# Performance work log

Measured on AMD Instinct MI355X. Metric: run time of the kernel, lower is better.

## Reference

```python
import jax, jax.numpy as jnp
import numpy as np

S, B, D_IN = 2048, 32, 512
H, PROJ, L = 1024, 512, 2
LN_EPS = 1e-5


def setup_inputs() -> dict:
    key = jax.random.key(0)
    ks = jax.random.split(key, 4)
    X = jax.random.normal(ks[0], (S, B, D_IN), dtype=jnp.float32)
    W = jax.random.normal(ks[1], (L, 3 * H, D_IN), dtype=jnp.float32) * (1.0 / np.sqrt(D_IN))
    b = jax.random.normal(ks[2], (L, 3 * H), dtype=jnp.float32) * 0.01
    P = jax.random.normal(ks[3], (L, PROJ, H), dtype=jnp.float32) * (1.0 / np.sqrt(H))
    gamma = jnp.ones((L, PROJ), dtype=jnp.float32)
    beta = jnp.zeros((L, PROJ), dtype=jnp.float32)
    return {"X": X, "W": W, "b": b, "P": P, "gamma": gamma, "beta": beta}


def _forget_mult(F, Z):
    # h_t = f_t * z_t + (1 - f_t) * h_{t-1}, h_0 = 0  (ForgetMult, hidden=None)
    def step(c, fz):
        f, z = fz
        c = f * z + (1.0 - f) * c
        return c, c
    c0 = jnp.zeros_like(Z[0])
    _, C = jax.lax.scan(step, c0, (F, Z))
    return C  # (S, B, H)


def _layer_norm(x, g, be):
    mu = jnp.mean(x, axis=-1, keepdims=True)
    var = jnp.mean(jnp.square(x - mu), axis=-1, keepdims=True)
    return (x - mu) * jax.lax.rsqrt(var + LN_EPS) * g + be


def reference(X, W, b, P, gamma, beta):
    inp = X
    last_states = []
    for i in range(L):
        # linear: (S,B,in) @ (in,3H) + b  -> gates
        Y = jnp.einsum('sbd,gd->sbg', inp, W[i]) + b[i]
        Z, F, O = jnp.split(Y, 3, axis=-1)
        Z = jnp.tanh(Z)
        F = jax.nn.sigmoid(F)
        C = _forget_mult(F, Z)                      # (S,B,H)
        Hout = jax.nn.sigmoid(O) * C                # output gate (QRNN-fo)
        inp = jnp.einsum('sbh,ph->sbp', Hout, P[i])  # projection, no bias
        inp = _layer_norm(inp, gamma[i], beta[i])
        last_states.append(C[-1])                   # (B,H)
    next_hidden = jnp.stack(last_states, axis=0)     # (L,B,H)
    return inp, next_hidden
```

## Files before the change

kernel.cpp:

```cpp
#include <hip/hip_runtime.h>
#include <hip/hip_bf16.h>

typedef _Float16 f16x8 __attribute__((ext_vector_type(8)));
typedef _Float16 f16x4 __attribute__((ext_vector_type(4)));
typedef float f32x4 __attribute__((ext_vector_type(4)));

#define SEQ 2048
#define BATCH 32
#define DIN 512
#define HID 1024
#define PROJ 512
#define ROWS (SEQ*BATCH)
#define G3H (3*HID)
#define NSEG 16
#define NCHAIN (BATCH*HID)

#define AS1(p) ((const __attribute__((address_space(1))) void*)(p))
#define AS3(p) ((__attribute__((address_space(3))) void*)(p))

__global__ __launch_bounds__(256)
void cvt_f32_f16(const float* __restrict__ in, _Float16* __restrict__ out, int n4)
{
    int i = blockIdx.x * 256 + threadIdx.x;
    if (i >= n4) return;
    float4 v = ((const float4*)in)[i];
    f16x4 o;
    o[0] = (_Float16)v.x; o[1] = (_Float16)v.y;
    o[2] = (_Float16)v.z; o[3] = (_Float16)v.w;
    ((f16x4*)out)[i] = o;
}

template<int MODE>
__global__ __launch_bounds__(256)
void gemm_lds(const _Float16* __restrict__ A, const _Float16* __restrict__ Bm,
              const float* __restrict__ bias, _Float16* __restrict__ C,
              int N, int K, int HH)
{
    __shared__ __align__(16) _Float16 sA[2][128][32];
    __shared__ __align__(16) _Float16 sB[2][128][32];

    const int tid  = threadIdx.x;
    const int lane = tid & 63;
    const int wave = tid >> 6;
    const int wm = wave >> 1;
    const int wn = wave & 1;
    const size_t row0 = (size_t)blockIdx.y * 128;
    const size_t col0 = (size_t)blockIdx.x * 128;

    const int crow = lane >> 2;
    const int ccol = (lane & 3) * 8;

    f32x4 acc[4][4] = {};

    const int rl = lane & 15;
    const int kb = (lane >> 4) * 8;
    const int nk = K / 32;

    const int c0 = wave * 2, c1 = wave * 2 + 1;
    const _Float16* gA0 = A  + (row0 + c0 * 16 + crow) * (size_t)K + ccol;
    const _Float16* gA1 = A  + (row0 + c1 * 16 + crow) * (size_t)K + ccol;
    const _Float16* gB0 = Bm + (col0 + c0 * 16 + crow) * (size_t)K + ccol;
    const _Float16* gB1 = Bm + (col0 + c1 * 16 + crow) * (size_t)K + ccol;

#define STAGE(buf, kt)                                                          \
    do {                                                                        \
        __builtin_amdgcn_global_load_lds(AS1(gA0 + (size_t)(kt) * 32),          \
                                         AS3(&sA[buf][c0 * 16][0]), 16, 0, 0);  \
        __builtin_amdgcn_global_load_lds(AS1(gB0 + (size_t)(kt) * 32),          \
                                         AS3(&sB[buf][c0 * 16][0]), 16, 0, 0);  \
        __builtin_amdgcn_global_load_lds(AS1(gA1 + (size_t)(kt) * 32),          \
                                         AS3(&sA[buf][c1 * 16][0]), 16, 0, 0);  \
        __builtin_amdgcn_global_load_lds(AS1(gB1 + (size_t)(kt) * 32),          \
                                         AS3(&sB[buf][c1 * 16][0]), 16, 0, 0);  \
    } while (0)

    int cur = 0;
    STAGE(0, 0);
    __syncthreads();

    for (int kt = 0; kt < nk; ++kt) {
        if (kt + 1 < nk) STAGE(cur ^ 1, kt + 1);
        f16x8 af[4], bf[4];
#pragma unroll
        for (int m = 0; m < 4; ++m)
            af[m] = *(const f16x8*)&sA[cur][wm * 64 + m * 16 + rl][kb];
#pragma unroll
        for (int n = 0; n < 4; ++n)
            bf[n] = *(const f16x8*)&sB[cur][wn * 64 + n * 16 + rl][kb];
#pragma unroll
        for (int m = 0; m < 4; ++m)
#pragma unroll
            for (int n = 0; n < 4; ++n)
                acc[m][n] = __builtin_amdgcn_mfma_f32_16x16x32_f16(af[m], bf[n], acc[m][n], 0, 0, 0);
        __syncthreads();
        cur ^= 1;
    }
#undef STAGE

#pragma unroll
    for (int m = 0; m < 4; ++m) {
#pragma unroll
        for (int n = 0; n < 4; ++n) {
            const size_t col = col0 + wn * 64 + n * 16 + rl;
            const size_t row = row0 + wm * 64 + m * 16 + (lane >> 4) * 4;
            float bv = (MODE == 0) ? bias[col] : 0.f;
#pragma unroll
            for (int j = 0; j < 4; ++j) {
                float v = acc[m][n][j];
                if (MODE == 0) {
                    v += bv;
                    if ((int)col < HH) {
                        float vc = fminf(fmaxf(v, -15.f), 15.f);
                        float e = __expf(2.f * vc);
                        v = __fdividef(e - 1.f, e + 1.f);
                    } else {
                        v = __fdividef(1.f, 1.f + __expf(-v));
                    }
                }
                C[(row + j) * (size_t)N + col] = (_Float16)v;
            }
        }
    }
}


__global__ __launch_bounds__(256)
void scan_p1(const _Float16* __restrict__ Y, float* __restrict__ Aseg,
             float* __restrict__ Bseg, int SL)
{
    const int t = blockIdx.x * 256 + threadIdx.x;
    const int g = blockIdx.y;
    const int h = t & (HID - 1);
    const int b = t >> 10;
    const _Float16* pz = Y + ((size_t)(g * SL) * BATCH + b) * G3H + h;
    const size_t strideY = (size_t)BATCH * G3H;
    float A = 1.f, Bv = 0.f;
#pragma unroll 4
    for (int k = 0; k < SL; ++k) {
        float z = (float)pz[0];
        float f = (float)pz[HID];
        Bv = f * z + (1.f - f) * Bv;
        A *= (1.f - f);
        pz += strideY;
    }
    Aseg[(size_t)g * NCHAIN + t] = A;
    Bseg[(size_t)g * NCHAIN + t] = Bv;
}

__global__ __launch_bounds__(256)
void scan_mid(const float* __restrict__ Aseg, const float* __restrict__ Bseg,
              float* __restrict__ cst, float* __restrict__ carry,
              float* __restrict__ hid, int first)
{
    const int t = blockIdx.x * 256 + threadIdx.x;
    float c = first ? 0.f : carry[t];
#pragma unroll
    for (int g = 0; g < NSEG; ++g) {
        cst[(size_t)g * NCHAIN + t] = c;
        c = Bseg[(size_t)g * NCHAIN + t] + Aseg[(size_t)g * NCHAIN + t] * c;
    }
    carry[t] = c;
    if (hid) hid[t] = c;
}

__global__ __launch_bounds__(256)
void scan_p2(const _Float16* __restrict__ Y, const float* __restrict__ cst,
             _Float16* __restrict__ Ho, int SL)
{
    const int t = blockIdx.x * 256 + threadIdx.x;
    const int g = blockIdx.y;
    const int h = t & (HID - 1);
    const int b = t >> 10;
    const _Float16* pz = Y + ((size_t)(g * SL) * BATCH + b) * G3H + h;
    _Float16* po = Ho + ((size_t)(g * SL) * BATCH + b) * HID + h;
    const size_t strideY = (size_t)BATCH * G3H;
    const size_t strideH = (size_t)BATCH * HID;
    float c = cst[(size_t)g * NCHAIN + t];
#pragma unroll 4
    for (int k = 0; k < SL; ++k) {
        float z = (float)pz[0];
        float f = (float)pz[HID];
        float o = (float)pz[2 * HID];
        c = f * z + (1.f - f) * c;
        *po = (_Float16)(o * c);
        pz += strideY;
        po += strideH;
    }
}

template<int OUT32>
__global__ __launch_bounds__(256)
void ln_kernel(const _Float16* __restrict__ Xin, const float* __restrict__ g,
               const float* __restrict__ be, _Float16* __restrict__ o16,
               float* __restrict__ o32)
{
    const int row  = blockIdx.x * 4 + (threadIdx.x >> 6);
    const int lane = threadIdx.x & 63;
    const _Float16* p = Xin + (size_t)row * PROJ + lane * 8;
    f16x8 v = *(const f16x8*)p;
    float x[8];
    float s = 0.f;
#pragma unroll
    for (int j = 0; j < 8; ++j) { x[j] = (float)v[j]; s += x[j]; }
#pragma unroll
    for (int d = 1; d < 64; d <<= 1) s += __shfl_xor(s, d);
    const float mu = s * (1.f / PROJ);
    float s2 = 0.f;
#pragma unroll
    for (int j = 0; j < 8; ++j) { float dd = x[j] - mu; s2 += dd * dd; }
#pragma unroll
    for (int d = 1; d < 64; d <<= 1) s2 += __shfl_xor(s2, d);
    const float rstd = rsqrtf(s2 * (1.f / PROJ) + 1e-5f);

    float y[8];
#pragma unroll
    for (int j = 0; j < 8; ++j)
        y[j] = (x[j] - mu) * rstd * g[lane * 8 + j] + be[lane * 8 + j];

    if (OUT32) {
        float* q = o32 + (size_t)row * PROJ + lane * 8;
        ((float4*)q)[0] = make_float4(y[0], y[1], y[2], y[3]);
        ((float4*)q)[1] = make_float4(y[4], y[5], y[6], y[7]);
    } else {
        f16x8 o;
#pragma unroll
        for (int j = 0; j < 8; ++j) o[j] = (_Float16)y[j];
        *(f16x8*)(o16 + (size_t)row * PROJ + lane * 8) = o;
    }
}

extern "C" void kernel_launch(void* const* d_in, const int* in_sizes, int n_in,
                              void* d_out, int out_size, void* d_ws, size_t ws_size,
                              hipStream_t stream)
{
    const float* X     = (const float*)d_in[0];
    const float* W     = (const float*)d_in[1];
    const float* b     = (const float*)d_in[2];
    const float* P     = (const float*)d_in[3];
    const float* gamma = (const float*)d_in[4];
    const float* beta  = (const float*)d_in[5];
    float* out = (float*)d_out;

    char* w = (char*)d_ws;
    _Float16* Xh = (_Float16*)w; w += (size_t)ROWS * DIN * 2;
    _Float16* Wh = (_Float16*)w; w += (size_t)2 * G3H * DIN * 2;
    _Float16* Ph = (_Float16*)w; w += (size_t)2 * PROJ * HID * 2;
    float* carry = (float*)w;    w += (size_t)NCHAIN * 4;
    float* Aseg  = (float*)w;    w += (size_t)NSEG * NCHAIN * 4;
    float* Bseg  = (float*)w;    w += (size_t)NSEG * NCHAIN * 4;
    float* cst   = (float*)w;    w += (size_t)NSEG * NCHAIN * 4;
    const size_t fixed = (size_t)(w - (char*)d_ws);

    const int cands[7] = {2048, 1024, 512, 256, 128, 64, 32};
    int CS = 32;
    for (int i = 0; i < 7; ++i) {
        size_t need = fixed + (size_t)cands[i] * 32 * (G3H + HID + PROJ) * 2;
        if (need <= ws_size) { CS = cands[i]; break; }
    }
    _Float16* Yg = (_Float16*)w; w += (size_t)CS * 32 * G3H * 2;
    _Float16* Ho = (_Float16*)w; w += (size_t)CS * 32 * HID * 2;
    _Float16* G2 = (_Float16*)w;

    cvt_f32_f16<<<(ROWS * DIN / 4 + 255) / 256, 256, 0, stream>>>(X, Xh, ROWS * DIN / 4);
    cvt_f32_f16<<<(2 * G3H * DIN / 4 + 255) / 256, 256, 0, stream>>>(W, Wh, 2 * G3H * DIN / 4);
    cvt_f32_f16<<<(2 * PROJ * HID / 4 + 255) / 256, 256, 0, stream>>>(P, Ph, 2 * PROJ * HID / 4);

    float* hid = out + (size_t)ROWS * PROJ;
    const int nch = SEQ / CS;
    const int rows = CS * BATCH;
    const int SL = CS / NSEG;

    for (int i = 0; i < 2; ++i) {
        for (int ch = 0; ch < nch; ++ch) {
            const size_t r0 = (size_t)ch * rows;
            gemm_lds<0><<<dim3(G3H / 128, rows / 128), 256, 0, stream>>>(
                Xh + r0 * DIN, Wh + (size_t)i * G3H * DIN, b + i * G3H, Yg, G3H, DIN, HID);
            scan_p1<<<dim3(NCHAIN / 256, NSEG), 256, 0, stream>>>(Yg, Aseg, Bseg, SL);
            scan_mid<<<NCHAIN / 256, 256, 0, stream>>>(
                Aseg, Bseg, cst, carry,
                (ch == nch - 1) ? hid + (size_t)i * NCHAIN : nullptr, ch == 0);
            scan_p2<<<dim3(NCHAIN / 256, NSEG), 256, 0, stream>>>(Yg, cst, Ho, SL);
            gemm_lds<1><<<dim3(PROJ / 128, rows / 128), 256, 0, stream>>>(
                Ho, Ph + (size_t)i * PROJ * HID, nullptr, G2, PROJ, HID, 0);
            if (i == 0)
                ln_kernel<0><<<rows / 4, 256, 0, stream>>>(G2, gamma, beta, Xh + r0 * PROJ, nullptr);
            else
                ln_kernel<1><<<rows / 4, 256, 0, stream>>>(G2, gamma + PROJ, beta + PROJ, nullptr, out + r0 * PROJ);
        }
    }
}
```

Baseline: 1.590 ms.

## Rework GEMM into 256x128 tiles with triple-buffered swizzled LDS pipeline

```diff
diff --git a/kernel.cpp b/kernel.cpp
--- a/kernel.cpp
+++ b/kernel.cpp
@@ -31,78 +31,117 @@
 }
 
 template<int MODE>
-__global__ __launch_bounds__(256)
+__global__ __launch_bounds__(512)
 void gemm_lds(const _Float16* __restrict__ A, const _Float16* __restrict__ Bm,
               const float* __restrict__ bias, _Float16* __restrict__ C,
               int N, int K, int HH)
 {
-    __shared__ __align__(16) _Float16 sA[2][128][32];
-    __shared__ __align__(16) _Float16 sB[2][128][32];
+    extern __shared__ __align__(16) char smem[];
+    char* sA = smem;
+    char* sB = smem + 98304;
 
     const int tid  = threadIdx.x;
     const int lane = tid & 63;
     const int wave = tid >> 6;
-    const int wm = wave >> 1;
-    const int wn = wave & 1;
-    const size_t row0 = (size_t)blockIdx.y * 128;
+    const int wm = wave & 3;
+    const int wn = wave >> 2;
+    const size_t row0 = (size_t)blockIdx.y * 256;
     const size_t col0 = (size_t)blockIdx.x * 128;
-
-    const int crow = lane >> 2;
-    const int ccol = (lane & 3) * 8;
+    const size_t Kb = (size_t)K * 2;
+
+    const char* Ab = (const char*)A;
+    const char* Bb = (const char*)Bm;
+
+    const int rl = lane & 15;
+    const int g  = lane >> 4;
+    const int swz = (rl & 7) << 4;
+    const int c0 = (g * 16) ^ swz;
+    const int c1 = (64 + g * 16) ^ swz;
+    const int aBase = (wm * 64 + rl) * 128;
+    const int bBase = (wn * 64 + rl) * 128;
+
+    const int srow = tid >> 3;
+    const int scb  = ((tid & 7) * 16) ^ ((srow & 7) << 4);
 
     f32x4 acc[4][4] = {};
-
-    const int rl = lane & 15;
-    const int kb = (lane >> 4) * 8;
-    const int nk = K / 32;
-
-    const int c0 = wave * 2, c1 = wave * 2 + 1;
-    const _Float16* gA0 = A  + (row0 + c0 * 16 + crow) * (size_t)K + ccol;
-    const _Float16* gA1 = A  + (row0 + c1 * 16 + crow) * (size_t)K + ccol;
-    const _Float16* gB0 = Bm + (col0 + c0 * 16 + crow) * (size_t)K + ccol;
-    const _Float16* gB1 = Bm + (col0 + c1 * 16 + crow) * (size_t)K + ccol;
-
-#define STAGE(buf, kt)                                                          \
-    do {                                                                        \
-        __builtin_amdgcn_global_load_lds(AS1(gA0 + (size_t)(kt) * 32),          \
-                                         AS3(&sA[buf][c0 * 16][0]), 16, 0, 0);  \
-        __builtin_amdgcn_global_load_lds(AS1(gB0 + (size_t)(kt) * 32),          \
-                                         AS3(&sB[buf][c0 * 16][0]), 16, 0, 0);  \
-        __builtin_amdgcn_global_load_lds(AS1(gA1 + (size_t)(kt) * 32),          \
-                                         AS3(&sA[buf][c1 * 16][0]), 16, 0, 0);  \
-        __builtin_amdgcn_global_load_lds(AS1(gB1 + (size_t)(kt) * 32),          \
-                                         AS3(&sB[buf][c1 * 16][0]), 16, 0, 0);  \
-    } while (0)
-
-    int cur = 0;
-    STAGE(0, 0);
-    __syncthreads();
-
-    for (int kt = 0; kt < nk; ++kt) {
-        if (kt + 1 < nk) STAGE(cur ^ 1, kt + 1);
+    const int nk = K / 64;
+
+#define STAGE_A(bufi, kt)                                                        \
+    do { _Pragma("unroll")                                                       \
+    for (int r = 0; r < 4; ++r) {                                                \
+        const char* src = Ab + (row0 + r * 64 + srow) * Kb + (size_t)(kt) * 128 + scb; \
+        __builtin_amdgcn_global_load_lds(AS1(src),                               \
+            AS3(sA + (bufi) * 32768 + r * 8192 + wave * 1024), 16, 0, 0);        \
+    } } while (0)
+#define STAGE_B(bufi, kt)                                                        \
+    do { _Pragma("unroll")                                                       \
+    for (int r = 0; r < 2; ++r) {                                                \
+        const char* src = Bb + (col0 + r * 64 + srow) * Kb + (size_t)(kt) * 128 + scb; \
+        __builtin_amdgcn_global_load_lds(AS1(src),                               \
+            AS3(sB + (bufi) * 16384 + r * 8192 + wave * 1024), 16, 0, 0);        \
+    } } while (0)
+#define BAR() asm volatile("s_barrier" ::: "memory")
+#define LGKM0() do { asm volatile("s_waitcnt lgkmcnt(0)" ::: "memory");          \
+                     __builtin_amdgcn_sched_barrier(0); } while (0)
+
+    STAGE_A(0, 0); STAGE_B(0, 0);
+    STAGE_A(1, 1); STAGE_B(1, 1);
+    asm volatile("s_waitcnt vmcnt(6)" ::: "memory");
+    BAR();
+
+    int buf = 0;
+    for (int t = 0; t < nk; ++t) {
+        const int nbuf = (buf >= 1) ? buf - 1 : buf + 2;
         f16x8 af[4], bf[4];
 #pragma unroll
         for (int m = 0; m < 4; ++m)
-            af[m] = *(const f16x8*)&sA[cur][wm * 64 + m * 16 + rl][kb];
+            af[m] = *(const f16x8*)(sA + buf * 32768 + aBase + m * 2048 + c0);
 #pragma unroll
         for (int n = 0; n < 4; ++n)
-            bf[n] = *(const f16x8*)&sB[cur][wn * 64 + n * 16 + rl][kb];
+            bf[n] = *(const f16x8*)(sB + buf * 16384 + bBase + n * 2048 + c0);
+        if (t + 2 < nk) STAGE_A(nbuf, t + 2);
+        BAR();
+        LGKM0();
+        __builtin_amdgcn_s_setprio(1);
 #pragma unroll
         for (int m = 0; m < 4; ++m)
 #pragma unroll
             for (int n = 0; n < 4; ++n)
                 acc[m][n] = __builtin_amdgcn_mfma_f32_16x16x32_f16(af[m], bf[n], acc[m][n], 0, 0, 0);
-        __syncthreads();
-        cur ^= 1;
-    }
-#undef STAGE
+        __builtin_amdgcn_s_setprio(0);
+        BAR();
+#pragma unroll
+        for (int m = 0; m < 4; ++m)
+            af[m] = *(const f16x8*)(sA + buf * 32768 + aBase + m * 2048 + c1);
+#pragma unroll
+        for (int n = 0; n < 4; ++n)
+            bf[n] = *(const f16x8*)(sB + buf * 16384 + bBase + n * 2048 + c1);
+        if (t + 2 < nk) STAGE_B(nbuf, t + 2);
+        BAR();
+        LGKM0();
+        __builtin_amdgcn_s_setprio(1);
+#pragma unroll
+        for (int m = 0; m < 4; ++m)
+#pragma unroll
+            for (int n = 0; n < 4; ++n)
+                acc[m][n] = __builtin_amdgcn_mfma_f32_16x16x32_f16(af[m], bf[n], acc[m][n], 0, 0, 0);
+        __builtin_amdgcn_s_setprio(0);
+        if (t + 2 < nk)      { asm volatile("s_waitcnt vmcnt(6)" ::: "memory"); }
+        else if (t + 1 < nk) { asm volatile("s_waitcnt vmcnt(0)" ::: "memory"); }
+        BAR();
+        buf = (buf == 2) ? 0 : buf + 1;
+    }
+#undef STAGE_A
+#undef STAGE_B
+#undef BAR
+#undef LGKM0
 
 #pragma unroll
     for (int m = 0; m < 4; ++m) {
 #pragma unroll
         for (int n = 0; n < 4; ++n) {
             const size_t col = col0 + wn * 64 + n * 16 + rl;
-            const size_t row = row0 + wm * 64 + m * 16 + (lane >> 4) * 4;
+            const size_t row = row0 + wm * 64 + m * 16 + g * 4;
             float bv = (MODE == 0) ? bias[col] : 0.f;
 #pragma unroll
             for (int j = 0; j < 4; ++j) {
@@ -241,6 +280,11 @@
     const float* beta  = (const float*)d_in[5];
     float* out = (float*)d_out;
 
+    (void)hipFuncSetAttribute((const void*)&gemm_lds<0>,
+                              hipFuncAttributeMaxDynamicSharedMemorySize, 147456);
+    (void)hipFuncSetAttribute((const void*)&gemm_lds<1>,
+                              hipFuncAttributeMaxDynamicSharedMemorySize, 147456);
+
     char* w = (char*)d_ws;
     _Float16* Xh = (_Float16*)w; w += (size_t)ROWS * DIN * 2;
     _Float16* Wh = (_Float16*)w; w += (size_t)2 * G3H * DIN * 2;
@@ -273,14 +317,14 @@
     for (int i = 0; i < 2; ++i) {
         for (int ch = 0; ch < nch; ++ch) {
             const size_t r0 = (size_t)ch * rows;
-            gemm_lds<0><<<dim3(G3H / 128, rows / 128), 256, 0, stream>>>(
+            gemm_lds<0><<<dim3(G3H / 128, rows / 256), 512, 147456, stream>>>(
                 Xh + r0 * DIN, Wh + (size_t)i * G3H * DIN, b + i * G3H, Yg, G3H, DIN, HID);
             scan_p1<<<dim3(NCHAIN / 256, NSEG), 256, 0, stream>>>(Yg, Aseg, Bseg, SL);
             scan_mid<<<NCHAIN / 256, 256, 0, stream>>>(
                 Aseg, Bseg, cst, carry,
                 (ch == nch - 1) ? hid + (size_t)i * NCHAIN : nullptr, ch == 0);
             scan_p2<<<dim3(NCHAIN / 256, NSEG), 256, 0, stream>>>(Yg, cst, Ho, SL);
-            gemm_lds<1><<<dim3(PROJ / 128, rows / 128), 256, 0, stream>>>(
+            gemm_lds<1><<<dim3(PROJ / 128, rows / 256), 512, 147456, stream>>>(
                 Ho, Ph + (size_t)i * PROJ * HID, nullptr, G2, PROJ, HID, 0);
             if (i == 0)
                 ln_kernel<0><<<rows / 4, 256, 0, stream>>>(G2, gamma, beta, Xh + r0 * PROJ, nullptr);
```

Result: no change. 1.617 ms (+1.7%).
